# Kernel optimization log

Hardware: AMD Instinct MI355X
Metric: run time of the kernel (lower is better)

## Reference

```python
import jax, jax.numpy as jnp
import numpy as np

RADIUS = 0.005
MAX_DEGREE = 32
N = 65536
S = 2048
INPUT_DIM = 32
HIDDEN = 256
NDIM = 1  # code requires ndim==1 for the add of pos-embed to projection


def sincos_embed(pos, dim):
    # pos: [N, ndim]; output [N, ndim*dim] (== [N, dim] for ndim=1), as in source
    half = dim // 2
    freq = jnp.exp(jnp.arange(half, dtype=pos.dtype) * (-jnp.log(10000.0) / (half - 1)))
    e = pos[:, :, None] * freq[None, None, :]          # [N, ndim, half]
    e = jnp.concatenate([jnp.sin(e), jnp.cos(e)], -1)  # [N, ndim, dim]
    return e.reshape(pos.shape[0], -1)


def setup_inputs() -> dict:
    key = jax.random.key(0)
    ks = jax.random.split(key, 8)
    inp = {
        "input_feat": jax.random.normal(ks[0], (N, INPUT_DIM), jnp.float32),
        "input_pos": jax.random.uniform(ks[1], (N, NDIM), jnp.float32),
        "supernode_idxs": jnp.arange(S, dtype=jnp.int32),
        "batch_idx": jnp.zeros((N,), jnp.int32),
        # LinearProjection (input proj), lecun_normal-like init
        "proj_W": jax.random.normal(ks[2], (INPUT_DIM, HIDDEN), jnp.float32) / np.sqrt(INPUT_DIM),
        "proj_b": jnp.zeros((HIDDEN,), jnp.float32),
        # message MLP: Dense(2H->H), gelu, Dense(H->H)
        "msg_W1": jax.random.normal(ks[3], (2 * HIDDEN, HIDDEN), jnp.float32) / np.sqrt(2 * HIDDEN),
        "msg_b1": jnp.zeros((HIDDEN,), jnp.float32),
        "msg_W2": jax.random.normal(ks[4], (HIDDEN, HIDDEN), jnp.float32) / np.sqrt(HIDDEN),
        "msg_b2": jnp.zeros((HIDDEN,), jnp.float32),
    }
    return inp


def reference(input_feat, input_pos, supernode_idxs, batch_idx,
              proj_W, proj_b, msg_W1, msg_b1, msg_W2, msg_b2):
    # node embedding: linear projection + continuous sincos positional embed
    x = input_feat @ proj_W + proj_b + sincos_embed(input_pos, HIDDEN)  # [N, H]

    # radius graph restricted to edges whose dst is a supernode:
    # per supernode, take up to MAX_DEGREE nearest neighbors within RADIUS (self-loop allowed)
    sup_pos = input_pos[supernode_idxs]                                  # [S, ndim]
    d2 = jnp.sum((sup_pos[:, None, :] - input_pos[None, :, :]) ** 2, -1)  # [S, N]
    neg_d2, nbr = jax.lax.top_k(-d2, MAX_DEGREE)                          # [S, K]
    within = (-neg_d2) <= RADIUS * RADIUS                                 # [S, K] mask

    x_src = x[nbr]                                                        # [S, K, H]
    x_dst = jnp.broadcast_to(x[supernode_idxs][:, None, :], x_src.shape) # [S, K, H]
    m_in = jnp.concatenate([x_src, x_dst], axis=-1)                       # [S, K, 2H]
    h = jax.nn.gelu(m_in @ msg_W1 + msg_b1)
    m = h @ msg_W2 + msg_b2                                               # [S, K, H]

    # segment mean over each supernode's in-radius edges
    w = within[..., None].astype(m.dtype)
    pooled = jnp.sum(m * w, axis=1) / jnp.maximum(jnp.sum(w, axis=1), 1.0)  # [S, H]
    return pooled[None]  # [batch_size=1, S, H]
```

## Files before the change

### kernel.cpp

```cpp
#include <hip/hip_runtime.h>
#include <hip/hip_bf16.h>
#include <float.h>

#define N_NODES 65536
#define S_SUP   2048
#define HDIM    256
#define KNN     32
#define NBINS   4096
#define CAP     4096
#define GSUP    2

typedef __attribute__((ext_vector_type(8))) __bf16 bf16x8;
typedef __attribute__((ext_vector_type(4))) float  f32x4;

__global__ __launch_bounds__(256) void embed_kernel(
        const float* __restrict__ feat, const float* __restrict__ pos,
        const float* __restrict__ W, const float* __restrict__ b,
        __hip_bfloat16* __restrict__ xb) {
    __shared__ float sf[64][32];
    __shared__ float sp[64];
    int tid = threadIdx.x;
    int rb = blockIdx.x * 64;
    {
        int r = tid >> 2, kg = tid & 3;
        const float* src = feat + (size_t)(rb + r) * 32 + kg * 8;
        float4 v0 = *(const float4*)(src);
        float4 v1 = *(const float4*)(src + 4);
        *(float4*)&sf[r][kg * 8]     = v0;
        *(float4*)&sf[r][kg * 8 + 4] = v1;
    }
    if (tid < 64) sp[tid] = pos[rb + tid];
    int c = tid;
    float wcol[32];
#pragma unroll
    for (int k = 0; k < 32; ++k) wcol[k] = W[k * 256 + c];
    float bias = b[c];
    const float coef = -logf(10000.0f) / 127.0f;
    float fr = expf((float)(c & 127) * coef);
    bool is_sin = (c < 128);
    __syncthreads();
    for (int r = 0; r < 64; ++r) {
        float acc = bias;
#pragma unroll
        for (int k = 0; k < 32; ++k) acc = fmaf(sf[r][k], wcol[k], acc);
        float e = sp[r] * fr;
        acc += is_sin ? __sinf(e) : __cosf(e);
        xb[(size_t)(rb + r) * 256 + c] = __float2bfloat16(acc);
    }
}

__global__ void transpose_w1_kernel(const float* __restrict__ W1, __hip_bfloat16* __restrict__ w1f) {
    int tile = blockIdx.x;
    int ks = tile >> 4, ntg = tile & 15;
    int tid = threadIdx.x;
    for (int i = tid; i < 512; i += 256) {
        int l = i >> 3, e = i & 7;
        int n = ntg * 16 + (l & 15);
        int k = ks * 32 + ((l >> 4) << 3) + e;
        w1f[(size_t)tile * 512 + i] = __float2bfloat16(W1[(size_t)k * 256 + n]);
    }
}

__device__ __forceinline__ int pos_bin(float p) {
    int b = (int)(p * (float)NBINS);
    return min(max(b, 0), NBINS - 1);
}

__global__ void hist_kernel(const float* __restrict__ pos, int* __restrict__ bin_cnt) {
    int n = blockIdx.x * blockDim.x + threadIdx.x;
    atomicAdd(&bin_cnt[pos_bin(pos[n])], 1);
}

__global__ void scan_kernel(const int* __restrict__ bin_cnt, int* __restrict__ bin_ofs,
                            int* __restrict__ cursor) {
    __shared__ int sdata[1024];
    int t = threadIdx.x;
    int v[4]; int s = 0;
#pragma unroll
    for (int i = 0; i < 4; ++i) { v[i] = bin_cnt[t * 4 + i]; s += v[i]; }
    sdata[t] = s;
    __syncthreads();
    for (int off = 1; off < 1024; off <<= 1) {
        int add = (t >= off) ? sdata[t - off] : 0;
        __syncthreads();
        sdata[t] += add;
        __syncthreads();
    }
    int run = sdata[t] - s;
#pragma unroll
    for (int i = 0; i < 4; ++i) {
        bin_ofs[t * 4 + i] = run;
        cursor[t * 4 + i]  = run;
        run += v[i];
    }
    if (t == 1023) bin_ofs[NBINS] = run;
}

__global__ void scatter_kernel(const float* __restrict__ pos, int* __restrict__ cursor,
                               int* __restrict__ sidx, float* __restrict__ spos) {
    int n = blockIdx.x * blockDim.x + threadIdx.x;
    float p = pos[n];
    int b = pos_bin(p);
    int dst = atomicAdd(&cursor[b], 1);
    sidx[dst] = n;
    spos[dst] = p;
}

__global__ void topk_kernel(const float* __restrict__ pos, const int* __restrict__ sup,
                            const int* __restrict__ bin_ofs, const int* __restrict__ sidx,
                            const float* __restrict__ spos,
                            int* __restrict__ nbr, int* __restrict__ within,
                            int* __restrict__ ncnt) {
    __shared__ float cd2[CAP];
    __shared__ int   cidx[CAP];
    __shared__ float rd2[KNN];
    __shared__ int   ridx[KNN];
    int s = blockIdx.x;
    int lane = threadIdx.x;
    float p = pos[sup[s]];
    int hb = pos_bin(p);
    const float BINW = 1.0f / (float)NBINS;
    int ccnt = 0;
    for (int r = 2;; r <<= 1) {
        int lo = max(hb - r, 0), hi = min(hb + r, NBINS - 1);
        int start = bin_ofs[lo], end = bin_ofs[hi + 1];
        ccnt = min(end - start, CAP);
        for (int i = lane; i < ccnt; i += 64) {
            float pp = spos[start + i];
            float d = p - pp;
            cd2[i] = d * d;
            cidx[i] = sidx[start + i];
        }
        __syncthreads();
        float gl = (lo == 0) ? FLT_MAX : (p - (float)lo * BINW);
        float gr = (hi == NBINS - 1) ? FLT_MAX : ((float)(hi + 1) * BINW - p);
        float g = fminf(gl, gr);
        float g2 = (g >= FLT_MAX) ? FLT_MAX : (g * 0.999f) * (g * 0.999f);
        int cw = 0;
        for (int i = lane; i < ccnt; i += 64) cw += (cd2[i] < g2) ? 1 : 0;
        for (int o = 32; o; o >>= 1) cw += __shfl_xor(cw, o);
        if (cw >= KNN || (lo == 0 && hi == NBINS - 1)) break;
        __syncthreads();
    }
    for (int t = 0; t < KNN; ++t) {
        unsigned long long best = ~0ULL;
        int bslot = -1;
        for (int i = lane; i < ccnt; i += 64) {
            unsigned long long k =
                ((unsigned long long)__float_as_uint(cd2[i]) << 32) | (unsigned)cidx[i];
            if (k < best) { best = k; bslot = i; }
        }
        unsigned long long mybest = best;
        for (int o = 32; o; o >>= 1) {
            unsigned long long other = __shfl_xor(best, o);
            best = best < other ? best : other;
        }
        if (mybest == best && bslot >= 0) cd2[bslot] = FLT_MAX;
        if (lane == 0) {
            rd2[t]  = __uint_as_float((unsigned)(best >> 32));
            ridx[t] = (int)(unsigned)(best & 0xffffffffULL);
        }
        __syncthreads();
    }
    const float R2 = (float)(0.005 * 0.005);
    if (lane < KNN) {
        float d2v = rd2[lane];
        int w = (d2v <= R2) ? 1 : 0;
        nbr[s * KNN + lane] = ridx[lane];
        within[s * KNN + lane] = w;
        unsigned long long m = __ballot(w != 0);
        int cnt = __popcll(m & 0xffffffffULL);
        if (lane == 0) ncnt[s] = cnt;
    }
}

__device__ __forceinline__ float gelu_tanh(float v) {
    float v3 = v * v * v;
    float t = tanhf(0.7978845608028654f * (v + 0.044715f * v3));
    return 0.5f * v * (1.0f + t);
}

__global__ __launch_bounds__(256) void edge_mlp_pool_kernel(
        const __hip_bfloat16* __restrict__ xb_,
        const __hip_bfloat16* __restrict__ w1f_,
        const float* __restrict__ b1,
        const int* __restrict__ sup,
        const int* __restrict__ nbr, const int* __restrict__ within,
        const int* __restrict__ ncnt, float* __restrict__ mh) {
    const ushort* xb  = (const ushort*)xb_;
    const ushort* w1f = (const ushort*)w1f_;
    int s0 = blockIdx.x * GSUP;
    int tid = threadIdx.x;
    int l = tid & 63, w = tid >> 6;
    int lr = l & 15, lg = l >> 4;
    __shared__ int snbr[GSUP][KNN];
    __shared__ int swin[GSUP][KNN];
    __shared__ int ssup[GSUP];
    if (tid < GSUP * KNN) {
        int g = tid >> 5, j = tid & 31;
        snbr[g][j] = nbr[(s0 + g) * KNN + j];
        swin[g][j] = within[(s0 + g) * KNN + j];
    }
    if (tid < GSUP) ssup[tid] = sup[s0 + tid];
    __syncthreads();
    const ushort* ar0[GSUP];
    const ushort* ar1[GSUP];
    const ushort* asp[GSUP];
#pragma unroll
    for (int g = 0; g < GSUP; ++g) {
        ar0[g] = xb + (size_t)snbr[g][lr]      * 256;
        ar1[g] = xb + (size_t)snbr[g][16 + lr] * 256;
        asp[g] = xb + (size_t)ssup[g]          * 256;
    }
    int koff = lg * 8;
    f32x4 acc[GSUP][2][4] = {};
#pragma unroll 1
    for (int ks = 0; ks < 8; ++ks) {
        int k = ks * 32 + koff;
        bf16x8 bfr[4];
#pragma unroll
        for (int nt = 0; nt < 4; ++nt)
            bfr[nt] = *(const bf16x8*)(w1f + ((size_t)(ks * 16 + w * 4 + nt) * 64 + l) * 8);
#pragma unroll
        for (int g = 0; g < GSUP; ++g) {
            bf16x8 a0 = *(const bf16x8*)(ar0[g] + k);
            bf16x8 a1 = *(const bf16x8*)(ar1[g] + k);
#pragma unroll
            for (int nt = 0; nt < 4; ++nt) {
                acc[g][0][nt] = __builtin_amdgcn_mfma_f32_16x16x32_bf16(a0, bfr[nt], acc[g][0][nt], 0, 0, 0);
                acc[g][1][nt] = __builtin_amdgcn_mfma_f32_16x16x32_bf16(a1, bfr[nt], acc[g][1][nt], 0, 0, 0);
            }
        }
    }
#pragma unroll 1
    for (int ks = 8; ks < 16; ++ks) {
        int k = (ks - 8) * 32 + koff;
        bf16x8 bfr[4];
#pragma unroll
        for (int nt = 0; nt < 4; ++nt)
            bfr[nt] = *(const bf16x8*)(w1f + ((size_t)(ks * 16 + w * 4 + nt) * 64 + l) * 8);
#pragma unroll
        for (int g = 0; g < GSUP; ++g) {
            bf16x8 a = *(const bf16x8*)(asp[g] + k);
#pragma unroll
            for (int nt = 0; nt < 4; ++nt) {
                acc[g][0][nt] = __builtin_amdgcn_mfma_f32_16x16x32_bf16(a, bfr[nt], acc[g][0][nt], 0, 0, 0);
                acc[g][1][nt] = __builtin_amdgcn_mfma_f32_16x16x32_bf16(a, bfr[nt], acc[g][1][nt], 0, 0, 0);
            }
        }
    }
#pragma unroll
    for (int nt = 0; nt < 4; ++nt) {
        int col = w * 64 + nt * 16 + lr;
        float bb = b1[col];
#pragma unroll
        for (int g = 0; g < GSUP; ++g) {
            float msum = 0.f;
#pragma unroll
            for (int mt = 0; mt < 2; ++mt)
#pragma unroll
                for (int d = 0; d < 4; ++d) {
                    int row = mt * 16 + lg * 4 + d;
                    float v = acc[g][mt][nt][d] + bb;
                    float gl = gelu_tanh(v);
                    msum += swin[g][row] ? gl : 0.f;
                }
            msum += __shfl_xor(msum, 16);
            msum += __shfl_xor(msum, 32);
            if (lg == 0) {
                float inv = 1.0f / (float)max(ncnt[s0 + g], 1);
                mh[(size_t)(s0 + g) * 256 + col] = msum * inv;
            }
        }
    }
}

__global__ void gemm64_kernel(const float* __restrict__ A, const int* __restrict__ rowidx,
                              const float* __restrict__ B, const float* __restrict__ bias,
                              const int* __restrict__ ncnt, float* __restrict__ C, int ldc) {
    __shared__ float At[32][68];
    __shared__ float Bs[32][64];
    int tid = threadIdx.x;
    int rb = blockIdx.x * 64, cb = blockIdx.y * 64;
    int tx = tid & 15, ty = tid >> 4;
    float acc[4][4] = {};
    int lr = tid >> 2, kg = tid & 3;
    int arow = rowidx ? rowidx[rb + lr] : (rb + lr);
    const float* aptr = A + (size_t)arow * 256 + kg * 8;
    int k2 = tid >> 3, cg = tid & 7;
    const float* bptr = B + (size_t)k2 * 256 + cb + cg * 8;
    for (int kc = 0; kc < 256; kc += 32) {
        float4 a0 = *(const float4*)(aptr + kc);
        float4 a1 = *(const float4*)(aptr + kc + 4);
        float4 b0 = *(const float4*)(bptr + (size_t)kc * 256);
        float4 b1v = *(const float4*)(bptr + (size_t)kc * 256 + 4);
        At[kg * 8 + 0][lr] = a0.x; At[kg * 8 + 1][lr] = a0.y;
        At[kg * 8 + 2][lr] = a0.z; At[kg * 8 + 3][lr] = a0.w;
        At[kg * 8 + 4][lr] = a1.x; At[kg * 8 + 5][lr] = a1.y;
        At[kg * 8 + 6][lr] = a1.z; At[kg * 8 + 7][lr] = a1.w;
        *(float4*)&Bs[k2][cg * 8]     = b0;
        *(float4*)&Bs[k2][cg * 8 + 4] = b1v;
        __syncthreads();
#pragma unroll
        for (int k = 0; k < 32; ++k) {
            float4 av = *(const float4*)&At[k][ty * 4];
            float4 bv = *(const float4*)&Bs[k][tx * 4];
            float a[4] = {av.x, av.y, av.z, av.w};
            float bb[4] = {bv.x, bv.y, bv.z, bv.w};
#pragma unroll
            for (int i = 0; i < 4; ++i)
#pragma unroll
                for (int j = 0; j < 4; ++j)
                    acc[i][j] = fmaf(a[i], bb[j], acc[i][j]);
        }
        __syncthreads();
    }
#pragma unroll
    for (int i = 0; i < 4; ++i) {
        int row = rb + ty * 4 + i;
        float bv[4] = {0.f, 0.f, 0.f, 0.f};
        if (bias) {
            float sc = ncnt ? ((ncnt[row] > 0) ? 1.0f : 0.0f) : 1.0f;
#pragma unroll
            for (int j = 0; j < 4; ++j) bv[j] = sc * bias[cb + tx * 4 + j];
        }
        float4 o;
        o.x = acc[i][0] + bv[0]; o.y = acc[i][1] + bv[1];
        o.z = acc[i][2] + bv[2]; o.w = acc[i][3] + bv[3];
        *(float4*)(C + (size_t)row * ldc + cb + tx * 4) = o;
    }
}

extern "C" void kernel_launch(void* const* d_in, const int* in_sizes, int n_in,
                              void* d_out, int out_size, void* d_ws, size_t ws_size,
                              hipStream_t stream) {
    const float* feat  = (const float*)d_in[0];
    const float* pos   = (const float*)d_in[1];
    const int*   sup   = (const int*)d_in[2];
    const float* projW = (const float*)d_in[4];
    const float* projb = (const float*)d_in[5];
    const float* W1    = (const float*)d_in[6];
    const float* b1    = (const float*)d_in[7];
    const float* W2    = (const float*)d_in[8];
    const float* b2    = (const float*)d_in[9];
    float* out = (float*)d_out;

    char* p = (char*)d_ws;
    auto alloc = [&](size_t bytes) { char* q = p; p += (bytes + 255) & ~255ULL; return q; };
    __hip_bfloat16* xb  = (__hip_bfloat16*)alloc((size_t)N_NODES * HDIM * 2);
    __hip_bfloat16* w1f = (__hip_bfloat16*)alloc((size_t)256 * 512 * 2);
    float* mh     = (float*)alloc((size_t)S_SUP * HDIM * 4);
    int*   sidx   = (int*)alloc((size_t)N_NODES * 4);
    float* spos   = (float*)alloc((size_t)N_NODES * 4);
    int*   nbr    = (int*)alloc((size_t)S_SUP * KNN * 4);
    int*   within = (int*)alloc((size_t)S_SUP * KNN * 4);
    int*   ncnt   = (int*)alloc((size_t)S_SUP * 4);
    int*   bin_cnt = (int*)alloc((size_t)NBINS * 4);
    int*   cursor  = (int*)alloc((size_t)NBINS * 4);
    int*   bin_ofs = (int*)alloc((size_t)(NBINS + 1) * 4);

    size_t needed = (size_t)(p - (char*)d_ws);
    if (needed > ws_size) {
        hipMemsetAsync(d_out, 0, (size_t)out_size * 4, stream);
        return;
    }

    hipMemsetAsync(bin_cnt, 0, (size_t)NBINS * 4, stream);
    embed_kernel<<<N_NODES / 64, 256, 0, stream>>>(feat, pos, projW, projb, xb);
    transpose_w1_kernel<<<256, 256, 0, stream>>>(W1, w1f);
    hist_kernel<<<N_NODES / 256, 256, 0, stream>>>(pos, bin_cnt);
    scan_kernel<<<1, 1024, 0, stream>>>(bin_cnt, bin_ofs, cursor);
    scatter_kernel<<<N_NODES / 256, 256, 0, stream>>>(pos, cursor, sidx, spos);
    topk_kernel<<<S_SUP, 64, 0, stream>>>(pos, sup, bin_ofs, sidx, spos, nbr, within, ncnt);
    edge_mlp_pool_kernel<<<S_SUP / GSUP, 256, 0, stream>>>(xb, w1f, b1, sup, nbr, within, ncnt, mh);
    gemm64_kernel<<<dim3(S_SUP / 64, 4), 256, 0, stream>>>(mh, nullptr, W2, b2, ncnt, out, 256);
}
```

Measured before the change: 218.8 us.

## Run output GEMM on bf16 MFMA and use a cheaper GELU

Replaces the fp32 scalar-FMA tiled GEMM for the second message-MLP layer with a bf16 MFMA kernel. W2 is transposed and converted into a fragment layout in the existing weight-prep kernel, and the pooled hidden values are written as bf16. The tanh-based GELU is rewritten as x*sigmoid(2u) using a fast exp and a hardware reciprocal. Together these cut ALU and memory traffic in the last stages, at the cost of bf16 rounding on the pooled activations and small approximation error in GELU.

Result: faster. 201.7 us (-7.8%).

```diff
diff --git a/kernel.cpp b/kernel.cpp
--- a/kernel.cpp
+++ b/kernel.cpp
@@ -49,15 +49,19 @@
     }
 }
 
-__global__ void transpose_w1_kernel(const float* __restrict__ W1, __hip_bfloat16* __restrict__ w1f) {
+__global__ void transpose_w_kernel(const float* __restrict__ W1, const float* __restrict__ W2,
+                                   __hip_bfloat16* __restrict__ w1f, __hip_bfloat16* __restrict__ w2f) {
     int tile = blockIdx.x;
-    int ks = tile >> 4, ntg = tile & 15;
     int tid = threadIdx.x;
+    const float* W = (tile < 256) ? W1 : W2;
+    __hip_bfloat16* dst = (tile < 256) ? w1f : w2f;
+    int t = (tile < 256) ? tile : (tile - 256);
+    int ks = t >> 4, ntg = t & 15;
     for (int i = tid; i < 512; i += 256) {
         int l = i >> 3, e = i & 7;
         int n = ntg * 16 + (l & 15);
         int k = ks * 32 + ((l >> 4) << 3) + e;
-        w1f[(size_t)tile * 512 + i] = __float2bfloat16(W1[(size_t)k * 256 + n]);
+        dst[(size_t)t * 512 + i] = __float2bfloat16(W[(size_t)k * 256 + n]);
     }
 }
 
@@ -174,10 +178,10 @@
     }
 }
 
-__device__ __forceinline__ float gelu_tanh(float v) {
-    float v3 = v * v * v;
-    float t = tanhf(0.7978845608028654f * (v + 0.044715f * v3));
-    return 0.5f * v * (1.0f + t);
+__device__ __forceinline__ float gelu_fast(float v) {
+    float u = 0.7978845608028654f * (v + 0.044715f * v * v * v);
+    float e = __expf(-2.0f * u);
+    return v * __builtin_amdgcn_rcpf(1.0f + e);
 }
 
 __global__ __launch_bounds__(256) void edge_mlp_pool_kernel(
@@ -186,7 +190,7 @@
         const float* __restrict__ b1,
         const int* __restrict__ sup,
         const int* __restrict__ nbr, const int* __restrict__ within,
-        const int* __restrict__ ncnt, float* __restrict__ mh) {
+        const int* __restrict__ ncnt, __hip_bfloat16* __restrict__ mhb) {
     const ushort* xb  = (const ushort*)xb_;
     const ushort* w1f = (const ushort*)w1f_;
     int s0 = blockIdx.x * GSUP;
@@ -262,72 +266,59 @@
                 for (int d = 0; d < 4; ++d) {
                     int row = mt * 16 + lg * 4 + d;
                     float v = acc[g][mt][nt][d] + bb;
-                    float gl = gelu_tanh(v);
+                    float gl = gelu_fast(v);
                     msum += swin[g][row] ? gl : 0.f;
                 }
             msum += __shfl_xor(msum, 16);
             msum += __shfl_xor(msum, 32);
             if (lg == 0) {
                 float inv = 1.0f / (float)max(ncnt[s0 + g], 1);
-                mh[(size_t)(s0 + g) * 256 + col] = msum * inv;
+                mhb[(size_t)(s0 + g) * 256 + col] = __float2bfloat16(msum * inv);
             }
         }
     }
 }
 
-__global__ void gemm64_kernel(const float* __restrict__ A, const int* __restrict__ rowidx,
-                              const float* __restrict__ B, const float* __restrict__ bias,
-                              const int* __restrict__ ncnt, float* __restrict__ C, int ldc) {
-    __shared__ float At[32][68];
-    __shared__ float Bs[32][64];
+__global__ __launch_bounds__(256) void out_gemm_kernel(
+        const __hip_bfloat16* __restrict__ mhb_, const __hip_bfloat16* __restrict__ w2f_,
+        const float* __restrict__ b2, const int* __restrict__ ncnt, float* __restrict__ out) {
+    const ushort* mhb = (const ushort*)mhb_;
+    const ushort* w2f = (const ushort*)w2f_;
+    int rb = blockIdx.x * 32;
     int tid = threadIdx.x;
-    int rb = blockIdx.x * 64, cb = blockIdx.y * 64;
-    int tx = tid & 15, ty = tid >> 4;
-    float acc[4][4] = {};
-    int lr = tid >> 2, kg = tid & 3;
-    int arow = rowidx ? rowidx[rb + lr] : (rb + lr);
-    const float* aptr = A + (size_t)arow * 256 + kg * 8;
-    int k2 = tid >> 3, cg = tid & 7;
-    const float* bptr = B + (size_t)k2 * 256 + cb + cg * 8;
-    for (int kc = 0; kc < 256; kc += 32) {
-        float4 a0 = *(const float4*)(aptr + kc);
-        float4 a1 = *(const float4*)(aptr + kc + 4);
-        float4 b0 = *(const float4*)(bptr + (size_t)kc * 256);
-        float4 b1v = *(const float4*)(bptr + (size_t)kc * 256 + 4);
-        At[kg * 8 + 0][lr] = a0.x; At[kg * 8 + 1][lr] = a0.y;
-        At[kg * 8 + 2][lr] = a0.z; At[kg * 8 + 3][lr] = a0.w;
-        At[kg * 8 + 4][lr] = a1.x; At[kg * 8 + 5][lr] = a1.y;
-        At[kg * 8 + 6][lr] = a1.z; At[kg * 8 + 7][lr] = a1.w;
-        *(float4*)&Bs[k2][cg * 8]     = b0;
-        *(float4*)&Bs[k2][cg * 8 + 4] = b1v;
-        __syncthreads();
-#pragma unroll
-        for (int k = 0; k < 32; ++k) {
-            float4 av = *(const float4*)&At[k][ty * 4];
-            float4 bv = *(const float4*)&Bs[k][tx * 4];
-            float a[4] = {av.x, av.y, av.z, av.w};
-            float bb[4] = {bv.x, bv.y, bv.z, bv.w};
-#pragma unroll
-            for (int i = 0; i < 4; ++i)
-#pragma unroll
-                for (int j = 0; j < 4; ++j)
-                    acc[i][j] = fmaf(a[i], bb[j], acc[i][j]);
-        }
-        __syncthreads();
-    }
-#pragma unroll
-    for (int i = 0; i < 4; ++i) {
-        int row = rb + ty * 4 + i;
-        float bv[4] = {0.f, 0.f, 0.f, 0.f};
-        if (bias) {
-            float sc = ncnt ? ((ncnt[row] > 0) ? 1.0f : 0.0f) : 1.0f;
-#pragma unroll
-            for (int j = 0; j < 4; ++j) bv[j] = sc * bias[cb + tx * 4 + j];
-        }
-        float4 o;
-        o.x = acc[i][0] + bv[0]; o.y = acc[i][1] + bv[1];
-        o.z = acc[i][2] + bv[2]; o.w = acc[i][3] + bv[3];
-        *(float4*)(C + (size_t)row * ldc + cb + tx * 4) = o;
+    int l = tid & 63, w = tid >> 6;
+    int lr = l & 15, lg = l >> 4;
+    const ushort* ar0 = mhb + (size_t)(rb + lr) * 256;
+    const ushort* ar1 = mhb + (size_t)(rb + 16 + lr) * 256;
+    int koff = lg * 8;
+    f32x4 acc[2][4] = {};
+#pragma unroll 1
+    for (int ks = 0; ks < 8; ++ks) {
+        int k = ks * 32 + koff;
+        bf16x8 bfr[4];
+#pragma unroll
+        for (int nt = 0; nt < 4; ++nt)
+            bfr[nt] = *(const bf16x8*)(w2f + ((size_t)(ks * 16 + w * 4 + nt) * 64 + l) * 8);
+        bf16x8 a0 = *(const bf16x8*)(ar0 + k);
+        bf16x8 a1 = *(const bf16x8*)(ar1 + k);
+#pragma unroll
+        for (int nt = 0; nt < 4; ++nt) {
+            acc[0][nt] = __builtin_amdgcn_mfma_f32_16x16x32_bf16(a0, bfr[nt], acc[0][nt], 0, 0, 0);
+            acc[1][nt] = __builtin_amdgcn_mfma_f32_16x16x32_bf16(a1, bfr[nt], acc[1][nt], 0, 0, 0);
+        }
+    }
+#pragma unroll
+    for (int nt = 0; nt < 4; ++nt) {
+        int col = w * 64 + nt * 16 + lr;
+        float bb = b2[col];
+#pragma unroll
+        for (int mt = 0; mt < 2; ++mt)
+#pragma unroll
+            for (int d = 0; d < 4; ++d) {
+                int row = rb + mt * 16 + lg * 4 + d;
+                float sc = (ncnt[row] > 0) ? 1.0f : 0.0f;
+                out[(size_t)row * 256 + col] = acc[mt][nt][d] + sc * bb;
+            }
     }
 }
 
@@ -349,7 +340,8 @@
     auto alloc = [&](size_t bytes) { char* q = p; p += (bytes + 255) & ~255ULL; return q; };
     __hip_bfloat16* xb  = (__hip_bfloat16*)alloc((size_t)N_NODES * HDIM * 2);
     __hip_bfloat16* w1f = (__hip_bfloat16*)alloc((size_t)256 * 512 * 2);
-    float* mh     = (float*)alloc((size_t)S_SUP * HDIM * 4);
+    __hip_bfloat16* w2f = (__hip_bfloat16*)alloc((size_t)128 * 512 * 2);
+    __hip_bfloat16* mhb = (__hip_bfloat16*)alloc((size_t)S_SUP * HDIM * 2);
     int*   sidx   = (int*)alloc((size_t)N_NODES * 4);
     float* spos   = (float*)alloc((size_t)N_NODES * 4);
     int*   nbr    = (int*)alloc((size_t)S_SUP * KNN * 4);
@@ -367,11 +359,11 @@
 
     hipMemsetAsync(bin_cnt, 0, (size_t)NBINS * 4, stream);
     embed_kernel<<<N_NODES / 64, 256, 0, stream>>>(feat, pos, projW, projb, xb);
-    transpose_w1_kernel<<<256, 256, 0, stream>>>(W1, w1f);
+    transpose_w_kernel<<<384, 256, 0, stream>>>(W1, W2, w1f, w2f);
     hist_kernel<<<N_NODES / 256, 256, 0, stream>>>(pos, bin_cnt);
     scan_kernel<<<1, 1024, 0, stream>>>(bin_cnt, bin_ofs, cursor);
     scatter_kernel<<<N_NODES / 256, 256, 0, stream>>>(pos, cursor, sidx, spos);
     topk_kernel<<<S_SUP, 64, 0, stream>>>(pos, sup, bin_ofs, sidx, spos, nbr, within, ncnt);
-    edge_mlp_pool_kernel<<<S_SUP / GSUP, 256, 0, stream>>>(xb, w1f, b1, sup, nbr, within, ncnt, mh);
-    gemm64_kernel<<<dim3(S_SUP / 64, 4), 256, 0, stream>>>(mh, nullptr, W2, b2, ncnt, out, 256);
-}
+    edge_mlp_pool_kernel<<<S_SUP / GSUP, 256, 0, stream>>>(xb, w1f, b1, sup, nbr, within, ncnt, mhb);
+    out_gemm_kernel<<<S_SUP / 32, 256, 0, stream>>>(mhb, w2f, b2, ncnt, out);
+}
```
